# Performance work log

Measured on AMD Instinct MI355X. Metric: run time of the kernel, lower is better.

Reference implementation:

```python
import jax, jax.numpy as jnp
import numpy as np

T, H, I, E = 2048, 2048, 1024, 16
TOP_K = 4

def setup_inputs() -> dict:
    key = jax.random.key(0)
    k1, k2, k3, k4, k5 = jax.random.split(key, 5)
    scale = 0.02
    return {
        "hidden_states": jax.random.normal(k1, (T, H), dtype=jnp.float32),
        "gate_w": jax.random.normal(k2, (E, H), dtype=jnp.float32) * scale,
        "w1": jax.random.normal(k3, (E, H, I), dtype=jnp.float32) * scale,  # gate proj
        "w3": jax.random.normal(k4, (E, H, I), dtype=jnp.float32) * scale,  # up proj
        "w2": jax.random.normal(k5, (E, I, H), dtype=jnp.float32) * scale,  # down proj
    }

def reference(hidden_states, gate_w, w1, w3, w2):
    # Router gate in fp32 (ReplicatedLinear, params_dtype=fp32, no bias)
    logits = hidden_states.astype(jnp.float32) @ gate_w.T          # [T, E]
    scores = jax.nn.softmax(logits, axis=-1)                        # scoring_func=softmax
    topk_w, topk_idx = jax.lax.top_k(scores, TOP_K)                 # [T, K]
    # renormalize=True, routed_scaling_factor=1.0
    topk_w = topk_w / jnp.sum(topk_w, axis=-1, keepdims=True)
    # Dense combine weights [T, E]: zero for non-selected experts, so
    # the dense all-expert compute below is mathematically identical to
    # sparse dispatch + grouped GEMM + combine.
    tok = jnp.arange(T)[:, None]
    cw = jnp.zeros((T, E), jnp.float32).at[tok, topk_idx].add(topk_w)
    # SwiGLU expert MLPs
    h1 = jnp.einsum('th,ehi->eti', hidden_states, w1)               # [E, T, I]
    h3 = jnp.einsum('th,ehi->eti', hidden_states, w3)               # [E, T, I]
    h2 = jnp.einsum('eti,eih->eth', jax.nn.silu(h1) * h3, w2)       # [E, T, H]
    out = jnp.einsum('te,eth->th', cw.astype(hidden_states.dtype), h2)
    return out
```

## Files before the change

### kernel.cpp

```cpp
#include <hip/hip_runtime.h>
#include <hip/hip_bf16.h>
#include <math.h>

#define T_TOK 2048
#define H_DIM 2048
#define I_DIM 1024
#define E_NUM 16
#define TOPK  4

#define BM 128
#define BN 128
#define BK 32

typedef __attribute__((ext_vector_type(8))) __bf16 bf16x8;
typedef __attribute__((ext_vector_type(4))) float  f32x4;

__device__ __forceinline__ unsigned short f2bf(float f) {
    unsigned int u = __builtin_bit_cast(unsigned int, f);
    unsigned int r = u + 0x7FFFu + ((u >> 16) & 1u);
    return (unsigned short)(r >> 16);
}

__device__ __forceinline__ void gload16(const void* g, void* l) {
    __builtin_amdgcn_global_load_lds(
        (const __attribute__((address_space(1))) unsigned int*)g,
        (__attribute__((address_space(3))) unsigned int*)l,
        16, 0, 0);
}

static const size_t WS_COUNTS  = 0;
static const size_t WS_OFFSETS = 256;
static const size_t WS_TOK     = 512;
static const size_t WS_WL      = 131584;
static const size_t WS_X16     = 262656;
static const size_t WS_W1T     = 8651264;
static const size_t WS_W3T     = 75760128;
static const size_t WS_W2T     = 142868992;
static const size_t WS_ACT     = 209977856;


__global__ void zero_init(float* __restrict__ out, int* __restrict__ counts) {
    int i = blockIdx.x * blockDim.x + threadIdx.x;
    ((float4*)out)[i] = make_float4(0.f, 0.f, 0.f, 0.f);
    if (i < E_NUM) counts[i] = 0;
}

__global__ void convert_x(const float* __restrict__ x, unsigned short* __restrict__ X16) {
    int i = blockIdx.x * blockDim.x + threadIdx.x;
    float4 v = ((const float4*)x)[i];
    ushort4 o;
    o.x = f2bf(v.x); o.y = f2bf(v.y); o.z = f2bf(v.z); o.w = f2bf(v.w);
    ((ushort4*)X16)[i] = o;
}

__global__ void transpose_conv(const float* __restrict__ in, unsigned short* __restrict__ out,
                               int R, int C) {
    __shared__ unsigned short tile[32][33];
    int e  = blockIdx.z;
    int c0 = blockIdx.x * 32;
    int r0 = blockIdx.y * 32;
    const float* ip = in + (size_t)e * R * C;
    unsigned short* op = out + (size_t)e * R * C;
    int t = threadIdx.x;
    int r  = t >> 3;
    int c4 = (t & 7) * 4;
    float4 v = *(const float4*)&ip[(size_t)(r0 + r) * C + c0 + c4];
    tile[c4 + 0][r] = f2bf(v.x);
    tile[c4 + 1][r] = f2bf(v.y);
    tile[c4 + 2][r] = f2bf(v.z);
    tile[c4 + 3][r] = f2bf(v.w);
    __syncthreads();
    ushort4 o;
    o.x = tile[r][c4 + 0];
    o.y = tile[r][c4 + 1];
    o.z = tile[r][c4 + 2];
    o.w = tile[r][c4 + 3];
    *(ushort4*)&op[(size_t)(c0 + r) * R + r0 + c4] = o;
}

__global__ void router(const float* __restrict__ x, const float* __restrict__ gw,
                       int* __restrict__ counts, int* __restrict__ tok,
                       float* __restrict__ wl) {
    int t = blockIdx.x;
    int lane = threadIdx.x;
    float acc[E_NUM];
#pragma unroll
    for (int e = 0; e < E_NUM; e++) acc[e] = 0.f;
    const float* xr = x + (size_t)t * H_DIM;
    for (int h = lane; h < H_DIM; h += 64) {
        float xv = xr[h];
#pragma unroll
        for (int e = 0; e < E_NUM; e++) acc[e] += xv * gw[e * H_DIM + h];
    }
#pragma unroll
    for (int e = 0; e < E_NUM; e++) {
#pragma unroll
        for (int off = 32; off; off >>= 1) acc[e] += __shfl_down(acc[e], off);
    }
    if (lane == 0) {
        bool used[E_NUM];
#pragma unroll
        for (int e = 0; e < E_NUM; e++) used[e] = false;
        int   idx[TOPK];
        float lv[TOPK];
        for (int k = 0; k < TOPK; k++) {
            float best = -1e30f; int bi = 0;
            for (int e = 0; e < E_NUM; e++)
                if (!used[e] && acc[e] > best) { best = acc[e]; bi = e; }
            used[bi] = true; idx[k] = bi; lv[k] = best;
        }
        float m = lv[0];
        float w[TOPK]; float s = 0.f;
        for (int k = 0; k < TOPK; k++) { w[k] = expf(lv[k] - m); s += w[k]; }
        float inv = 1.f / s;
        for (int k = 0; k < TOPK; k++) {
            int pos = atomicAdd(&counts[idx[k]], 1);
            tok[idx[k] * T_TOK + pos] = t;
            wl [idx[k] * T_TOK + pos] = w[k] * inv;
        }
    }
}

__global__ void prefix(const int* __restrict__ counts, int* __restrict__ offsets) {
    if (threadIdx.x == 0 && blockIdx.x == 0) {
        int s = 0;
        for (int e = 0; e < E_NUM; e++) { offsets[e] = s; s += counts[e]; }
    }
}

__global__ __launch_bounds__(256, 2) void stage1(
    const unsigned short* __restrict__ X16,
    const unsigned short* __restrict__ w1t,
    const unsigned short* __restrict__ w3t,
    const int* __restrict__ counts, const int* __restrict__ offsets,
    const int* __restrict__ tok, const float* __restrict__ wl,
    unsigned short* __restrict__ act)
{
    int e   = blockIdx.z;
    int n_e = counts[e];
    int m0  = blockIdx.y * BM;
    if (m0 >= n_e) return;
    int n0  = blockIdx.x * BN;

    __shared__ __align__(16) unsigned short As [BM][BK];
    __shared__ __align__(16) unsigned short B1s[BN][BK];
    __shared__ __align__(16) unsigned short B2s[BN][BK];

    int tid  = threadIdx.x;
    int wave = tid >> 6, lane = tid & 63;
    int wm = (wave >> 1) * 64, wn = (wave & 1) * 64;
    int lr = lane & 15, lq = lane >> 4;

    const unsigned short* w1p = w1t + (size_t)e * I_DIM * H_DIM;
    const unsigned short* w3p = w3t + (size_t)e * I_DIM * H_DIM;

    int ar[2]; int rr[2]; int cc[2];
#pragma unroll
    for (int rep = 0; rep < 2; rep++) {
        int idx = rep * 256 + tid;
        rr[rep] = idx >> 2;
        cc[rep] = (idx & 3) * 8;
        int gm = m0 + rr[rep];
        ar[rep] = tok[e * T_TOK + (gm < n_e ? gm : n_e - 1)];
    }

    f32x4 acc1[4][4] = {};
    f32x4 acc3[4][4] = {};

    for (int k0 = 0; k0 < H_DIM; k0 += BK) {
#pragma unroll
        for (int rep = 0; rep < 2; rep++) {
            int r = rr[rep], ch = cc[rep];
            gload16(&X16[(size_t)ar[rep] * H_DIM + k0 + ch], &As [r][ch]);
            gload16(&w1p[(size_t)(n0 + r) * H_DIM + k0 + ch], &B1s[r][ch]);
            gload16(&w3p[(size_t)(n0 + r) * H_DIM + k0 + ch], &B2s[r][ch]);
        }
        __syncthreads();
        bf16x8 af[4], b1f[4], b2f[4];
#pragma unroll
        for (int ti = 0; ti < 4; ti++)
            af[ti] = *(const bf16x8*)&As[wm + ti * 16 + lr][lq * 8];
#pragma unroll
        for (int tj = 0; tj < 4; tj++) {
            b1f[tj] = *(const bf16x8*)&B1s[wn + tj * 16 + lr][lq * 8];
            b2f[tj] = *(const bf16x8*)&B2s[wn + tj * 16 + lr][lq * 8];
        }
#pragma unroll
        for (int ti = 0; ti < 4; ti++)
#pragma unroll
            for (int tj = 0; tj < 4; tj++) {
                acc1[ti][tj] = __builtin_amdgcn_mfma_f32_16x16x32_bf16(af[ti], b1f[tj], acc1[ti][tj], 0, 0, 0);
                acc3[ti][tj] = __builtin_amdgcn_mfma_f32_16x16x32_bf16(af[ti], b2f[tj], acc3[ti][tj], 0, 0, 0);
            }
        __syncthreads();
    }

    int slotbase = offsets[e] + m0;
#pragma unroll
    for (int ti = 0; ti < 4; ti++) {
#pragma unroll
        for (int reg = 0; reg < 4; reg++) {
            int mrow = wm + ti * 16 + lq * 4 + reg;
            int gm = m0 + mrow;
            if (gm >= n_e) continue;
            float wt = wl[e * T_TOK + gm];
            size_t obase = (size_t)(slotbase + mrow) * I_DIM + n0;
#pragma unroll
            for (int tj = 0; tj < 4; tj++) {
                float h1 = acc1[ti][tj][reg];
                float h3 = acc3[ti][tj][reg];
                float a = (h1 / (1.f + expf(-h1))) * h3 * wt;
                act[obase + wn + tj * 16 + lr] = f2bf(a);
            }
        }
    }
}

__global__ __launch_bounds__(256, 2) void stage2(
    const unsigned short* __restrict__ act,
    const unsigned short* __restrict__ w2t,
    const int* __restrict__ counts, const int* __restrict__ offsets,
    const int* __restrict__ tok,
    float* __restrict__ out)
{
    int e   = blockIdx.z;
    int n_e = counts[e];
    int m0  = blockIdx.y * BM;
    if (m0 >= n_e) return;
    int n0  = blockIdx.x * BN;

    __shared__ __align__(16) unsigned short As[BM][BK];
    __shared__ __align__(16) unsigned short Bs[BN][BK];

    int tid  = threadIdx.x;
    int wave = tid >> 6, lane = tid & 63;
    int wm = (wave >> 1) * 64, wn = (wave & 1) * 64;
    int lr = lane & 15, lq = lane >> 4;

    const unsigned short* w2p = w2t + (size_t)e * H_DIM * I_DIM;
    int slotbase = offsets[e];

    int rr[2]; int cc[2]; int arow[2];
#pragma unroll
    for (int rep = 0; rep < 2; rep++) {
        int idx = rep * 256 + tid;
        rr[rep] = idx >> 2;
        cc[rep] = (idx & 3) * 8;
        int gm = m0 + rr[rep];
        arow[rep] = slotbase + (gm < n_e ? gm : n_e - 1);
    }

    f32x4 acc[4][4] = {};

    for (int k0 = 0; k0 < I_DIM; k0 += BK) {
#pragma unroll
        for (int rep = 0; rep < 2; rep++) {
            int r = rr[rep], ch = cc[rep];
            gload16(&act[(size_t)arow[rep] * I_DIM + k0 + ch], &As[r][ch]);
            gload16(&w2p[(size_t)(n0 + r) * I_DIM + k0 + ch], &Bs[r][ch]);
        }
        __syncthreads();
        bf16x8 af[4], bf[4];
#pragma unroll
        for (int ti = 0; ti < 4; ti++)
            af[ti] = *(const bf16x8*)&As[wm + ti * 16 + lr][lq * 8];
#pragma unroll
        for (int tj = 0; tj < 4; tj++)
            bf[tj] = *(const bf16x8*)&Bs[wn + tj * 16 + lr][lq * 8];
#pragma unroll
        for (int ti = 0; ti < 4; ti++)
#pragma unroll
            for (int tj = 0; tj < 4; tj++)
                acc[ti][tj] = __builtin_amdgcn_mfma_f32_16x16x32_bf16(af[ti], bf[tj], acc[ti][tj], 0, 0, 0);
        __syncthreads();
    }

#pragma unroll
    for (int ti = 0; ti < 4; ti++) {
#pragma unroll
        for (int reg = 0; reg < 4; reg++) {
            int mrow = wm + ti * 16 + lq * 4 + reg;
            int gm = m0 + mrow;
            if (gm >= n_e) continue;
            int tm = tok[e * T_TOK + gm];
            size_t obase = (size_t)tm * H_DIM + n0;
#pragma unroll
            for (int tj = 0; tj < 4; tj++)
                atomicAdd(&out[obase + wn + tj * 16 + lr], acc[ti][tj][reg]);
        }
    }
}

extern "C" void kernel_launch(void* const* d_in, const int* in_sizes, int n_in,
                              void* d_out, int out_size, void* d_ws, size_t ws_size,
                              hipStream_t stream) {
    const float* x_f32 = (const float*)d_in[0];
    const float* gw    = (const float*)d_in[1];
    const float* w1    = (const float*)d_in[2];
    const float* w3    = (const float*)d_in[3];
    const float* w2    = (const float*)d_in[4];
    float* out = (float*)d_out;

    char* ws = (char*)d_ws;
    int*            counts  = (int*)(ws + WS_COUNTS);
    int*            offsets = (int*)(ws + WS_OFFSETS);
    int*            tok     = (int*)(ws + WS_TOK);
    float*          wl      = (float*)(ws + WS_WL);
    unsigned short* X16     = (unsigned short*)(ws + WS_X16);
    unsigned short* w1t     = (unsigned short*)(ws + WS_W1T);
    unsigned short* w3t     = (unsigned short*)(ws + WS_W3T);
    unsigned short* w2t     = (unsigned short*)(ws + WS_W2T);
    unsigned short* act     = (unsigned short*)(ws + WS_ACT);

    zero_init<<<dim3((T_TOK * H_DIM / 4) / 256), 256, 0, stream>>>(out, counts);
    convert_x<<<dim3((T_TOK * H_DIM / 4) / 256), 256, 0, stream>>>(x_f32, X16);
    transpose_conv<<<dim3(I_DIM / 32, H_DIM / 32, E_NUM), 256, 0, stream>>>(w1, w1t, H_DIM, I_DIM);
    transpose_conv<<<dim3(I_DIM / 32, H_DIM / 32, E_NUM), 256, 0, stream>>>(w3, w3t, H_DIM, I_DIM);
    transpose_conv<<<dim3(H_DIM / 32, I_DIM / 32, E_NUM), 256, 0, stream>>>(w2, w2t, I_DIM, H_DIM);
    router<<<dim3(T_TOK), 64, 0, stream>>>(x_f32, gw, counts, tok, wl);
    prefix<<<dim3(1), 64, 0, stream>>>(counts, offsets);
    stage1<<<dim3(I_DIM / BN, T_TOK / BM, E_NUM), 256, 0, stream>>>(
        X16, w1t, w3t, counts, offsets, tok, wl, act);
    stage2<<<dim3(H_DIM / BN, T_TOK / BM, E_NUM), 256, 0, stream>>>(
        act, w2t, counts, offsets, tok, out);
}
```

Measured before the change: 786.2 us.

## Double-buffer LDS tiles in both MoE GEMM stages to overlap loads with MFMA

Both grouped-GEMM kernels now keep two LDS buffers per operand. Each iteration issues the direct-to-LDS loads for the next K tile before running the MFMAs on the current one, and replaces the two __syncthreads with one vmcnt wait plus barrier at the end. This hides global load latency behind matrix math and removes one barrier per iteration. Launch bounds are also raised to 3 blocks per CU, which limits registers, while LDS use per block doubles. Stage1's large accumulator set could spill under the tighter register budget.

Measured after the change: 873.4 us. +11.1%, slower.

```diff
diff --git a/kernel.cpp b/kernel.cpp
--- a/kernel.cpp
+++ b/kernel.cpp
@@ -128,7 +128,7 @@
     }
 }
 
-__global__ __launch_bounds__(256, 2) void stage1(
+__global__ __launch_bounds__(256, 3) void stage1(
     const unsigned short* __restrict__ X16,
     const unsigned short* __restrict__ w1t,
     const unsigned short* __restrict__ w3t,
@@ -142,9 +142,9 @@
     if (m0 >= n_e) return;
     int n0  = blockIdx.x * BN;
 
-    __shared__ __align__(16) unsigned short As [BM][BK];
-    __shared__ __align__(16) unsigned short B1s[BN][BK];
-    __shared__ __align__(16) unsigned short B2s[BN][BK];
+    __shared__ __align__(16) unsigned short As [2][BM][BK];
+    __shared__ __align__(16) unsigned short B1s[2][BN][BK];
+    __shared__ __align__(16) unsigned short B2s[2][BN][BK];
 
     int tid  = threadIdx.x;
     int wave = tid >> 6, lane = tid & 63;
@@ -164,26 +164,35 @@
         ar[rep] = tok[e * T_TOK + (gm < n_e ? gm : n_e - 1)];
     }
 
+    auto stage = [&](int buf, int k0) {
+#pragma unroll
+        for (int rep = 0; rep < 2; rep++) {
+            int r = rr[rep], ch = cc[rep];
+            gload16(&X16[(size_t)ar[rep] * H_DIM + k0 + ch], &As [buf][r][ch]);
+            gload16(&w1p[(size_t)(n0 + r) * H_DIM + k0 + ch], &B1s[buf][r][ch]);
+            gload16(&w3p[(size_t)(n0 + r) * H_DIM + k0 + ch], &B2s[buf][r][ch]);
+        }
+    };
+
     f32x4 acc1[4][4] = {};
     f32x4 acc3[4][4] = {};
 
-    for (int k0 = 0; k0 < H_DIM; k0 += BK) {
-#pragma unroll
-        for (int rep = 0; rep < 2; rep++) {
-            int r = rr[rep], ch = cc[rep];
-            gload16(&X16[(size_t)ar[rep] * H_DIM + k0 + ch], &As [r][ch]);
-            gload16(&w1p[(size_t)(n0 + r) * H_DIM + k0 + ch], &B1s[r][ch]);
-            gload16(&w3p[(size_t)(n0 + r) * H_DIM + k0 + ch], &B2s[r][ch]);
-        }
-        __syncthreads();
+    const int NK = H_DIM / BK;
+    stage(0, 0);
+    asm volatile("s_waitcnt vmcnt(0)" ::: "memory");
+    __builtin_amdgcn_s_barrier();
+
+    for (int t = 0; t < NK; ++t) {
+        int cur = t & 1;
+        if (t + 1 < NK) stage(cur ^ 1, (t + 1) * BK);
         bf16x8 af[4], b1f[4], b2f[4];
 #pragma unroll
         for (int ti = 0; ti < 4; ti++)
-            af[ti] = *(const bf16x8*)&As[wm + ti * 16 + lr][lq * 8];
+            af[ti] = *(const bf16x8*)&As[cur][wm + ti * 16 + lr][lq * 8];
 #pragma unroll
         for (int tj = 0; tj < 4; tj++) {
-            b1f[tj] = *(const bf16x8*)&B1s[wn + tj * 16 + lr][lq * 8];
-            b2f[tj] = *(const bf16x8*)&B2s[wn + tj * 16 + lr][lq * 8];
+            b1f[tj] = *(const bf16x8*)&B1s[cur][wn + tj * 16 + lr][lq * 8];
+            b2f[tj] = *(const bf16x8*)&B2s[cur][wn + tj * 16 + lr][lq * 8];
         }
 #pragma unroll
         for (int ti = 0; ti < 4; ti++)
@@ -192,7 +201,8 @@
                 acc1[ti][tj] = __builtin_amdgcn_mfma_f32_16x16x32_bf16(af[ti], b1f[tj], acc1[ti][tj], 0, 0, 0);
                 acc3[ti][tj] = __builtin_amdgcn_mfma_f32_16x16x32_bf16(af[ti], b2f[tj], acc3[ti][tj], 0, 0, 0);
             }
-        __syncthreads();
+        asm volatile("s_waitcnt vmcnt(0)" ::: "memory");
+        __builtin_amdgcn_s_barrier();
     }
 
     int slotbase = offsets[e] + m0;
@@ -216,7 +226,7 @@
     }
 }
 
-__global__ __launch_bounds__(256, 2) void stage2(
+__global__ __launch_bounds__(256, 3) void stage2(
     const unsigned short* __restrict__ act,
     const unsigned short* __restrict__ w2t,
     const int* __restrict__ counts, const int* __restrict__ offsets,
@@ -229,8 +239,8 @@
     if (m0 >= n_e) return;
     int n0  = blockIdx.x * BN;
 
-    __shared__ __align__(16) unsigned short As[BM][BK];
-    __shared__ __align__(16) unsigned short Bs[BN][BK];
+    __shared__ __align__(16) unsigned short As[2][BM][BK];
+    __shared__ __align__(16) unsigned short Bs[2][BN][BK];
 
     int tid  = threadIdx.x;
     int wave = tid >> 6, lane = tid & 63;
@@ -250,29 +260,39 @@
         arow[rep] = slotbase + (gm < n_e ? gm : n_e - 1);
     }
 
-    f32x4 acc[4][4] = {};
-
-    for (int k0 = 0; k0 < I_DIM; k0 += BK) {
+    auto stage = [&](int buf, int k0) {
 #pragma unroll
         for (int rep = 0; rep < 2; rep++) {
             int r = rr[rep], ch = cc[rep];
-            gload16(&act[(size_t)arow[rep] * I_DIM + k0 + ch], &As[r][ch]);
-            gload16(&w2p[(size_t)(n0 + r) * I_DIM + k0 + ch], &Bs[r][ch]);
-        }
-        __syncthreads();
+            gload16(&act[(size_t)arow[rep] * I_DIM + k0 + ch], &As[buf][r][ch]);
+            gload16(&w2p[(size_t)(n0 + r) * I_DIM + k0 + ch], &Bs[buf][r][ch]);
+        }
+    };
+
+    f32x4 acc[4][4] = {};
+
+    const int NK = I_DIM / BK;
+    stage(0, 0);
+    asm volatile("s_waitcnt vmcnt(0)" ::: "memory");
+    __builtin_amdgcn_s_barrier();
+
+    for (int t = 0; t < NK; ++t) {
+        int cur = t & 1;
+        if (t + 1 < NK) stage(cur ^ 1, (t + 1) * BK);
         bf16x8 af[4], bf[4];
 #pragma unroll
         for (int ti = 0; ti < 4; ti++)
-            af[ti] = *(const bf16x8*)&As[wm + ti * 16 + lr][lq * 8];
+            af[ti] = *(const bf16x8*)&As[cur][wm + ti * 16 + lr][lq * 8];
 #pragma unroll
         for (int tj = 0; tj < 4; tj++)
-            bf[tj] = *(const bf16x8*)&Bs[wn + tj * 16 + lr][lq * 8];
+            bf[tj] = *(const bf16x8*)&Bs[cur][wn + tj * 16 + lr][lq * 8];
 #pragma unroll
         for (int ti = 0; ti < 4; ti++)
 #pragma unroll
             for (int tj = 0; tj < 4; tj++)
                 acc[ti][tj] = __builtin_amdgcn_mfma_f32_16x16x32_bf16(af[ti], bf[tj], acc[ti][tj], 0, 0, 0);
-        __syncthreads();
+        asm volatile("s_waitcnt vmcnt(0)" ::: "memory");
+        __builtin_amdgcn_s_barrier();
     }
 
 #pragma unroll
```
